# Performance work log

Measured on AMD Instinct MI355X. Metric: run time of the kernel, lower is better.

## Reference

```python
import jax, jax.numpy as jnp
import numpy as np
from jax import lax

DATA_NUM, CNUM, AUG_NUM, LNUM = 64, 6, 4, 3
B, H, W = 16, 512, 512
T_SEL = 0  # fixed aug selection (torch draws np.random.randint at runtime)
EPS = 1e-8
DN = ('NCHW', 'OIHW', 'NCHW')


def setup_inputs() -> dict:
    key = jax.random.key(0)
    ks = jax.random.split(key, 8)
    GLA_img_aug = jax.random.uniform(ks[0], (B, 1, H, W), dtype=jnp.float32)
    lbl = jax.random.randint(ks[1], (B, H, W), 0, CNUM, dtype=jnp.int32)
    index = jax.random.randint(ks[2], (B,), 0, DATA_NUM, dtype=jnp.int32)
    # learned params: Bezier control params (5+2=7 slots, only 0..3 used) and per-(sample,class,aug,layer) tiny conv pairs
    param = jax.random.uniform(ks[3], (DATA_NUM, CNUM, AUG_NUM, LNUM, 7), dtype=jnp.float32)
    w1 = 0.1 * jax.random.normal(ks[4], (DATA_NUM, CNUM, AUG_NUM, LNUM, 4, 1, 3, 3), dtype=jnp.float32)
    b1 = 0.01 * jax.random.normal(ks[5], (DATA_NUM, CNUM, AUG_NUM, LNUM, 4), dtype=jnp.float32)
    w2 = 0.1 * jax.random.normal(ks[6], (DATA_NUM, CNUM, AUG_NUM, LNUM, 1, 4, 3, 3), dtype=jnp.float32)
    b2 = 0.01 * jax.random.normal(ks[7], (DATA_NUM, CNUM, AUG_NUM, LNUM, 1), dtype=jnp.float32)
    return {"GLA_img_aug": GLA_img_aug, "lbl": lbl, "index": index,
            "param": param, "w1": w1, "b1": b1, "w2": w2, "b2": b2}


def _conv_pair(x, w1, b1, w2, b2):
    # x: [1,H,W]; per-sample Conv2d(1,4,3,p=1) -> Conv2d(4,1,3,p=1)
    y = lax.conv_general_dilated(x[None], w1, (1, 1), 'SAME', dimension_numbers=DN) + b1[None, :, None, None]
    y = lax.conv_general_dilated(y, w2, (1, 1), 'SAME', dimension_numbers=DN) + b2[None, :, None, None]
    return y[0]

_conv_batch = jax.vmap(_conv_pair)  # batched over per-sample weights


def _ftransfer(xn, lbl, i, index, param, w1, b1, w2, b2):
    raw = xn                                   # [B,1,H,W]
    mask = (lbl[:, None, :, :] == i)           # [B,1,H,W]
    c = xn * mask
    pp = jax.nn.sigmoid(param[index, i, T_SEL])   # [B,L,7]  (p := sigmoid)
    W1, B1 = w1[index, i, T_SEL], b1[index, i, T_SEL]
    W2, B2 = w2[index, i, T_SEL], b2[index, i, T_SEL]
    for layer in range(LNUM):
        p1 = pp[:, layer, 0][:, None, None, None]
        p2 = pp[:, layer, 1][:, None, None, None]
        p1v = pp[:, layer, 2][:, None, None, None]
        p2v = pp[:, layer, 3][:, None, None, None]
        mix = jax.nn.sigmoid(_conv_batch(raw, W1[:, layer], B1[:, layer], W2[:, layer], B2[:, layer]))
        om = 1.0 - c
        ct = 3.0 * om**2 * c * p1 + 3.0 * om * c**2 * p2 + c**3          # p0=0,  p3=1
        cv = om**3 + 3.0 * om**2 * c * p1v + 3.0 * om * c**2 * p2v       # p0v=1, p3v=0
        c = jnp.clip(ct * mix + cv * (1.0 - mix), 0.0, 1.0)
    # write back only where label == i (equivalent to torch's flag-filtered scatter)
    return jnp.where(mask, c, raw)


def reference(GLA_img_aug, lbl, index, param, w1, b1, w2, b2):
    x = GLA_img_aug
    mn = jnp.min(x, axis=(1, 2, 3), keepdims=True)
    mx = jnp.max(x, axis=(1, 2, 3), keepdims=True)
    scale = mx - mn + EPS
    xn = (x - mn) / scale
    for i in range(CNUM):
        xn = _ftransfer(xn, lbl, i, index, param, w1, b1, w2, b2)
    return xn * scale + mn
```

## Files before the change

kernel.cpp:

```cpp
#include <hip/hip_runtime.h>
#include <stdint.h>

#define HW 512
#define IMG (HW*HW)
#define CNUM_ 6

#define TILE 64
#define HALO 12
#define ST 88
#define SSTR 89
#define NT 512
#define RCAP 256

typedef float f2 __attribute__((ext_vector_type(2)));

#define LTOT 3840

#define RECBASE 2048
#define REC_F 96
#define VARBASE (RECBASE + 96*REC_F)
#define VAR_F 27

__global__ __launch_bounds__(256) void k_prep(const float4* __restrict__ x4,
                       const int* __restrict__ index, const float* __restrict__ param,
                       const float* __restrict__ w1, const float* __restrict__ b1,
                       const float* __restrict__ w2, const float* __restrict__ b2,
                       float* __restrict__ wsf){
    __shared__ float w1s[108], w2s[108], b1s[12], b2s[3], prm[21];
    __shared__ float smn[4], smx[4];
    const int r = blockIdx.x, t = threadIdx.x;
    if (r >= 96){
        int blk = r - 96;
        int base4 = blk * 1024;
        float vmin = 1e30f, vmax = -1e30f;
#pragma unroll
        for (int k = 0; k < 4; k++){
            float4 v = x4[base4 + k*256 + t];
            vmin = fminf(vmin, fminf(fminf(v.x, v.y), fminf(v.z, v.w)));
            vmax = fmaxf(vmax, fmaxf(fmaxf(v.x, v.y), fmaxf(v.z, v.w)));
        }
#pragma unroll
        for (int off = 32; off > 0; off >>= 1){
            vmin = fminf(vmin, __shfl_down(vmin, off));
            vmax = fmaxf(vmax, __shfl_down(vmax, off));
        }
        int wv = t >> 6;
        if ((t & 63) == 0){ smn[wv] = vmin; smx[wv] = vmax; }
        __syncthreads();
        if (t == 0){
            wsf[2*blk]     = fminf(fminf(smn[0], smn[1]), fminf(smn[2], smn[3]));
            wsf[2*blk + 1] = fmaxf(fmaxf(smx[0], smx[1]), fmaxf(smx[2], smx[3]));
        }
        return;
    }
    const int b = r / 6, i = r % 6;
    const int lb0 = (index[b]*CNUM_ + i) * 12;
    if (t < 108){
        int l = t / 36, j = t % 36;
        w1s[t] = w1[(lb0 + l)*36 + j];
        w2s[t] = w2[(lb0 + l)*36 + j];
    }
    if (t < 12) b1s[t] = b1[(lb0 + t/4)*4 + (t%4)];
    if (t < 3)  b2s[t] = b2[lb0 + t];
    if (t < 21) prm[t] = param[(lb0 + t/7)*7 + (t%7)];
    __syncthreads();
    float* rec = wsf + RECBASE + r*REC_F;
    float* var = wsf + VARBASE + r*9*3*VAR_F;
    for (int u = t; u < 9*3*26; u += 256){
        int kind = u / 78, rem = u % 78, l = rem / 26, e = rem % 26;
        int rowk = kind / 3, colk = kind % 3;
        if (e < 25){
            int ty = e/5 - 2, tx = e%5 - 2;
            float we = 0.f;
            for (int d = 0; d < 9; d++){
                int dy = d/3 - 1, dx = d%3 - 1;
                if ((rowk==0 && dy<0)||(rowk==2 && dy>0)||(colk==0 && dx<0)||(colk==2 && dx>0)) continue;
                int ey = ty - dy, ex = tx - dx;
                if (ey < -1 || ey > 1 || ex < -1 || ex > 1) continue;
                for (int c = 0; c < 4; c++)
                    we += w2s[l*36 + c*9 + d] * w1s[l*36 + c*9 + (ey+1)*3 + (ex+1)];
            }
            var[(kind*3 + l)*VAR_F + e] = we;
            if (kind == 4) rec[l*25 + e] = we;
        } else {
            float be = b2s[l];
            for (int c = 0; c < 4; c++){
                float sw = 0.f;
                for (int d = 0; d < 9; d++){
                    int dy = d/3 - 1, dx = d%3 - 1;
                    if ((rowk==0 && dy<0)||(rowk==2 && dy>0)||(colk==0 && dx<0)||(colk==2 && dx>0)) continue;
                    sw += w2s[l*36 + c*9 + d];
                }
                be += b1s[l*4 + c] * sw;
            }
            var[(kind*3 + l)*VAR_F + 25] = be;
            if (kind == 4) rec[75 + l] = be;
        }
    }
    if (t < 18){
        int l = t / 6, q = t % 6;
        float p1  = __builtin_amdgcn_rcpf(1.f + __expf(-prm[l*7 + 0]));
        float p2  = __builtin_amdgcn_rcpf(1.f + __expf(-prm[l*7 + 1]));
        float p1v = __builtin_amdgcn_rcpf(1.f + __expf(-prm[l*7 + 2]));
        float p2v = __builtin_amdgcn_rcpf(1.f + __expf(-prm[l*7 + 3]));
        float v;
        switch (q){
            case 0: v = 3.f*p1; break;
            case 1: v = 3.f*p2 - 6.f*p1; break;
            case 2: v = 1.f + 3.f*p1 - 3.f*p2; break;
            case 3: v = 3.f*p1v - 3.f; break;
            case 4: v = 3.f - 6.f*p1v + 3.f*p2v; break;
            default: v = -1.f + 3.f*p1v - 3.f*p2v; break;
        }
        rec[78 + l*6 + q] = v;
    }
}

__device__ __forceinline__ float sig1(float z){
    return __builtin_amdgcn_rcpf(1.f + __expf(-z));
}

__device__ __forceinline__ float bez3(float c, float mix, const float* __restrict__ cf){
    float ct = c * (cf[0] + c * (cf[1] + c * cf[2]));
    float cv = 1.f + c * (cf[3] + c * (cf[4] + c * cf[5]));
    float r = cv + mix * (ct - cv);
    return __builtin_amdgcn_fmed3f(r, 0.f, 1.f);
}

__device__ __forceinline__ f2 splat(float v){ f2 r = {v, v}; return r; }

__device__ __forceinline__ f2 sig2(f2 z){
    f2 r;
    r.x = __builtin_amdgcn_rcpf(1.f + __expf(-z.x));
    r.y = __builtin_amdgcn_rcpf(1.f + __expf(-z.y));
    return r;
}

__device__ __forceinline__ f2 bez3p(f2 c, f2 mix, const float* __restrict__ cf){
    f2 ct = c * (splat(cf[0]) + c * (splat(cf[1]) + c * splat(cf[2])));
    f2 cv = splat(1.f) + c * (splat(cf[3]) + c * (splat(cf[4]) + c * splat(cf[5])));
    f2 r = cv + mix * (ct - cv);
    r.x = __builtin_amdgcn_fmed3f(r.x, 0.f, 1.f);
    r.y = __builtin_amdgcn_fmed3f(r.y, 0.f, 1.f);
    return r;
}

__device__ __forceinline__ void load_taps(const float* __restrict__ s, int pos, float* tp){
    const float* sp0 = s + pos - (2*SSTR + 2);
    const float* sp1 = s + pos + (SSTR - 2);
#pragma unroll
    for (int wy = 0; wy < 3; wy++)
#pragma unroll
    for (int wx = 0; wx < 5; wx++)
        tp[wy*5 + wx] = sp0[wy*SSTR + wx];
#pragma unroll
    for (int wy = 0; wy < 2; wy++)
#pragma unroll
    for (int wx = 0; wx < 5; wx++)
        tp[15 + wy*5 + wx] = sp1[wy*SSTR + wx];
}

__device__ __forceinline__ void conv_px(const float* __restrict__ s, int pos,
                                        const float* __restrict__ rec,
                                        float& z0, float& z1, float& z2, float& cc){
    float tp[25];
    load_taps(s, pos, tp);
    f2 a0 = {rec[75], 0.f};
    f2 a1 = {rec[76], 0.f};
    f2 a2 = {rec[77], 0.f};
#pragma unroll
    for (int e = 0; e < 24; e += 2){
        f2 tv = {tp[e], tp[e+1]};
        f2 w0 = {rec[e],      rec[e+1]};
        f2 w1 = {rec[25 + e], rec[26 + e]};
        f2 w2 = {rec[50 + e], rec[51 + e]};
        a0 += w0 * tv;
        a1 += w1 * tv;
        a2 += w2 * tv;
    }
    float t24 = tp[24];
    z0 = a0.x + a0.y + rec[24]*t24;
    z1 = a1.x + a1.y + rec[49]*t24;
    z2 = a2.x + a2.y + rec[74]*t24;
    cc = tp[12];
}

__device__ __forceinline__ unsigned short* gl_addr(float* out, int sbase, int Y0, int X0, int e){
    return (unsigned short*)(out + sbase + (Y0 + HALO + (e >> 7))*HW + X0 + HALO) + (e & 127);
}

__device__ __forceinline__ void classify_px(int ce, unsigned short pos, int lane,
        int* cnt, unsigned short* lst, float* out, int sbase, int Y0, int X0){
    unsigned long long m0 = __ballot(ce & 1);
    unsigned long long m1 = __ballot(ce & 2);
    unsigned long long m2 = __ballot(ce & 4);
    int basev = 0;
    if (lane < 6){
        unsigned long long mc = ((lane & 1) ? m0 : ~m0)
                              & ((lane & 2) ? m1 : ~m1)
                              & ((lane & 4) ? m2 : ~m2);
        int pc = __popcll(mc);
        if (pc) basev = atomicAdd(&cnt[lane], pc);
    }
    int mybase = __shfl(basev, ce < 6 ? ce : 0);
    if (ce < 6){
        unsigned long long mself = ((ce & 1) ? m0 : ~m0)
                                 & ((ce & 2) ? m1 : ~m1)
                                 & ((ce & 4) ? m2 : ~m2);
        int p = mybase + __popcll(mself & ((1ull << lane) - 1ull));
        if (ce < 3){
            int capc = 1408 - (ce << 7);
            int offc = ce * (1472 - (ce << 6));
            if (p < capc) lst[offc + p] = pos;
        } else {
            int d = ce - 3;
            int capc = 1056 - 96*d;
            int offc = d * (1104 - 48*d);
            if (p < capc) *gl_addr(out, sbase, Y0, X0, offc + p) = pos;
        }
    }
}

__global__ __launch_bounds__(NT, 8) void k_main(
        const float* __restrict__ x, const int* __restrict__ lbl,
        float* __restrict__ out, const float* __restrict__ wsf){
    __shared__ float s[ST*SSTR];
    __shared__ unsigned short lst[LTOT];
    __shared__ unsigned rlst[RCAP];
    __shared__ int cnt[8];
    __shared__ float snorm[4];
    const int lin = ((blockIdx.z << 3) + blockIdx.y) * 8 + blockIdx.x;
    const int xcd = lin & 7;
    const int e = lin >> 3;
    int img2, idx;
    if (e < 56){
        int r = e >> 1; img2 = e & 1;
        if (r < 8)       idx = r;
        else if (r < 16) idx = 56 + (r - 8);
        else { int t = r - 16; idx = (1 + (t >> 1))*8 + (t & 1)*7; }
    } else {
        int f = e - 56; img2 = f & 1; int t = f >> 1;
        idx = (1 + t/6)*8 + 1 + t%6;
    }
    const int b = xcd*2 + img2;
    const int by = idx >> 3, bx = idx & 7;
    const int X0 = bx * TILE - HALO, Y0 = by * TILE - HALO;
    const int tid = threadIdx.x;
    const int lane = tid & 63;
    const int sbase = b * IMG;
    const bool edgeblk = (bx == 0) | (bx == 7) | (by == 0) | (by == 7);

    if (tid < 8) cnt[tid] = 0;
    if (tid < 64){
        float pmn = wsf[2*(b*64 + tid)];
        float pmx = wsf[2*(b*64 + tid) + 1];
#pragma unroll
        for (int off = 32; off > 0; off >>= 1){
            pmn = fminf(pmn, __shfl_down(pmn, off));
            pmx = fmaxf(pmx, __shfl_down(pmx, off));
        }
        if (tid == 0){
            float scv = pmx - pmn + 1e-8f;
            snorm[0] = pmn; snorm[1] = scv; snorm[2] = 1.0f / scv;
        }
    }
    __syncthreads();
    const float mn = snorm[0], sc = snorm[1], inv = snorm[2];
    const float mninv = mn * inv;

    {
        int q = tid << 2;
        int ly = q / ST, lx = q - ly*ST;
        int pbase = ly*SSTR + lx;
        for (int it = 0; it < 4; it++){
            bool act = (it < 3) | (tid < (ST*ST - 3*4*NT) / 4);
            int gy = Y0 + ly, gxb = X0 + lx;
            bool vq = act & ((unsigned)gy < (unsigned)HW) & ((unsigned)gxb <= (unsigned)(HW - 4));
            float4 xv = {0.f, 0.f, 0.f, 0.f};
            int4  lv = {255, 255, 255, 255};
            if (vq){
                int off = sbase + (gy << 9) + gxb;
                xv = *(const float4*)(x + off);
                lv = *(const int4*)(lbl + off);
                xv.x = xv.x*inv - mninv;
                xv.y = xv.y*inv - mninv;
                xv.z = xv.z*inv - mninv;
                xv.w = xv.w*inv - mninv;
            }
            if (act){
                s[pbase + 0] = xv.x;
                s[pbase + 1] = xv.y;
                s[pbase + 2] = xv.z;
                s[pbase + 3] = xv.w;
            }
            int mrow = min(ly, ST-1-ly);
#pragma unroll
            for (int j = 0; j < 4; j++){
                int c = (&lv.x)[j];
                int lxj = lx + j;
                int margin = min(min(lxj, ST-1-lxj), mrow);
                bool ringj = false;
                if (edgeblk){
                    int gxj = gxb + j;
                    ringj = vq & ((gxj==0) | (gxj==HW-1) | (gy==0) | (gy==HW-1));
                }
                int ce = (c < CNUM_ && !ringj && margin >= 2 + 2*c) ? c : 7;
                classify_px(ce, (unsigned short)(pbase + j), lane, cnt, lst, out, sbase, Y0, X0);
                if (edgeblk){
                    bool ringok = ringj && c < CNUM_ && margin >= 2;
                    unsigned long long rm = __ballot(ringok);
                    if (rm){
                        int base = 0;
                        if (lane == 0) base = atomicAdd(&cnt[6], __popcll(rm));
                        base = __shfl(base, 0);
                        if (ringok){
                            int p = base + __popcll(rm & ((1ull << lane) - 1ull));
                            if (p < RCAP) rlst[p] = ((unsigned)c << 16) | (unsigned)(pbase + j);
                        }
                    }
                }
            }
            lx += 24; ly += 23; pbase += 23*SSTR + 24;
            if (lx >= ST){ lx -= ST; ly += 1; pbase += SSTR - ST; }
        }
    }
    __syncthreads();
    const int rn = min(cnt[6], RCAP);

    unsigned short pf[9];
#pragma unroll
    for (int d = 0; d < 3; d++){
        int capc = 1056 - 96*d;
        int offc = d * (1104 - 48*d);
        int nB = min(cnt[3 + d], capc);
#pragma unroll
        for (int sl = 0; sl < 3; sl++){
            int j = tid + sl*NT;
            unsigned short pv = 0;
            if (j < nB) pv = *gl_addr(out, sbase, Y0, X0, offc + j);
            pf[d*3 + sl] = pv;
        }
    }

#pragma unroll
    for (int cls = 0; cls < CNUM_; cls++){
        const int capc = (cls < 3) ? (1408 - (cls << 7)) : (1056 - 96*(cls - 3));
        const float* rec = wsf + RECBASE + (b*CNUM_ + cls)*REC_F;
        const int n = min(cnt[cls], capc);
        const int j0 = tid, j1 = tid + NT, j2 = tid + 2*NT;
        const bool v0 = j0 < n, v1 = j1 < n, v2 = j2 < n;
        int p0 = 0, p1 = 0, p2 = 0;
        if (cls < 3){
            const unsigned short* lp = lst + cls * (1472 - (cls << 6));
            if (v0) p0 = lp[j0];
            if (v1) p1 = lp[j1];
            if (v2) p2 = lp[j2];
        } else {
            p0 = pf[(cls-3)*3 + 0];
            p1 = pf[(cls-3)*3 + 1];
            p2 = pf[(cls-3)*3 + 2];
        }
        __builtin_amdgcn_s_setprio(1);
        float z00=0.f, z01=0.f, z02=0.f, cc0=0.f;
        float z10=0.f, z11=0.f, z12=0.f, cc1=0.f;
        float u0, u1, u2;
        if (v0) conv_px(s, p0, rec, z00, z01, z02, cc0);
        if (v1) conv_px(s, p1, rec, z10, z11, z12, cc1);
        if (v0 | v1){
            f2 cP = {cc0, cc1};
            cP = bez3p(cP, sig2((f2){z00, z10}), rec + 78);
            cP = bez3p(cP, sig2((f2){z01, z11}), rec + 84);
            cP = bez3p(cP, sig2((f2){z02, z12}), rec + 90);
            u0 = cP.x; u1 = cP.y;
        }
        if (v2){
            float za, zb, zc, cc;
            conv_px(s, p2, rec, za, zb, zc, cc);
            cc = bez3(cc, sig1(za), rec + 78);
            cc = bez3(cc, sig1(zb), rec + 84);
            u2 = bez3(cc, sig1(zc), rec + 90);
        }
        __builtin_amdgcn_s_setprio(0);
        int hav = -1; float rupd = 0.f;
        if (edgeblk && tid < rn){
            unsigned ev = rlst[tid];
            int rc = (int)(ev >> 16), pos = (int)(ev & 0xffff);
            int ly = pos / SSTR, lx = pos % SSTR;
            int margin = min(min(lx, ST-1-lx), min(ly, ST-1-ly));
            if (rc == cls && margin >= 2 + 2*cls){
                int gy = Y0 + ly, gx = X0 + lx;
                int rowk = (gy == 0) ? 0 : ((gy == HW-1) ? 2 : 1);
                int colk = (gx == 0) ? 0 : ((gx == HW-1) ? 2 : 1);
                const float* vb = wsf + VARBASE + ((b*CNUM_ + cls)*9 + rowk*3 + colk)*3*VAR_F;
                float tp[25];
                load_taps(s, pos, tp);
                float c = tp[12];
#pragma unroll
                for (int l = 0; l < 3; l++){
                    float z = vb[l*VAR_F + 25];
#pragma unroll
                    for (int e2 = 0; e2 < 25; e2++) z += vb[l*VAR_F + e2] * tp[e2];
                    c = bez3(c, sig1(z), rec + 78 + 6*l);
                }
                rupd = c; hav = pos;
            }
        }
        __syncthreads();
        if (v0) s[p0] = u0;
        if (v1) s[p1] = u1;
        if (v2) s[p2] = u2;
        if (hav >= 0) s[hav] = rupd;
        __syncthreads();
    }

    for (int j = tid; j < TILE*TILE; j += NT){
        int py = j >> 6, px = j & 63;
        int gy = Y0 + HALO + py, gx = X0 + HALO + px;
        out[sbase + gy*HW + gx] = s[(HALO + py)*SSTR + (HALO + px)] * sc + mn;
    }
}

extern "C" void kernel_launch(void* const* d_in, const int* in_sizes, int n_in,
                              void* d_out, int out_size, void* d_ws, size_t ws_size,
                              hipStream_t stream){
    const float* x     = (const float*)d_in[0];
    const int*   lbl   = (const int*)  d_in[1];
    const int*   index = (const int*)  d_in[2];
    const float* param = (const float*)d_in[3];
    const float* w1    = (const float*)d_in[4];
    const float* b1    = (const float*)d_in[5];
    const float* w2    = (const float*)d_in[6];
    const float* b2    = (const float*)d_in[7];
    float* out = (float*)d_out;
    float* wsf = (float*)d_ws;

    k_prep<<<1120, 256, 0, stream>>>((const float4*)x, index, param, w1, b1, w2, b2, wsf);
    dim3 g(8, 8, 16);
    k_main<<<g, NT, 0, stream>>>(x, lbl, out, wsf);
}
```

Before: 164.1 us.

## Bucket class pixel lists by position mod 32 to get bank-conflict-free gathers

Replaces the ballot-based per-class compaction with a two-pass counting sort. Pixels are binned by class and (pos & 31), the bins are prefix-scanned, then scattered into the class lists, and each lane processes its own bucket. The intent is that lanes in a wave touch stencil positions on distinct LDS banks, cutting bank conflicts in conv_px. The paired f2 conv path is dropped, the RCAP ring buffer is shrunk, and the final store is vectorized to float4. In exchange it adds LDS atomics per pixel, an extra classification pass, and a wavefront loop of up to 6 iterations bounded by the largest bucket, which can cause load imbalance.

```diff
diff --git a/kernel.cpp b/kernel.cpp
--- a/kernel.cpp
+++ b/kernel.cpp
@@ -10,7 +10,7 @@
 #define ST 88
 #define SSTR 89
 #define NT 512
-#define RCAP 256
+#define RCAP 176
 
 typedef float f2 __attribute__((ext_vector_type(2)));
 
@@ -127,24 +127,6 @@
     return __builtin_amdgcn_fmed3f(r, 0.f, 1.f);
 }
 
-__device__ __forceinline__ f2 splat(float v){ f2 r = {v, v}; return r; }
-
-__device__ __forceinline__ f2 sig2(f2 z){
-    f2 r;
-    r.x = __builtin_amdgcn_rcpf(1.f + __expf(-z.x));
-    r.y = __builtin_amdgcn_rcpf(1.f + __expf(-z.y));
-    return r;
-}
-
-__device__ __forceinline__ f2 bez3p(f2 c, f2 mix, const float* __restrict__ cf){
-    f2 ct = c * (splat(cf[0]) + c * (splat(cf[1]) + c * splat(cf[2])));
-    f2 cv = splat(1.f) + c * (splat(cf[3]) + c * (splat(cf[4]) + c * splat(cf[5])));
-    f2 r = cv + mix * (ct - cv);
-    r.x = __builtin_amdgcn_fmed3f(r.x, 0.f, 1.f);
-    r.y = __builtin_amdgcn_fmed3f(r.y, 0.f, 1.f);
-    return r;
-}
-
 __device__ __forceinline__ void load_taps(const float* __restrict__ s, int pos, float* tp){
     const float* sp0 = s + pos - (2*SSTR + 2);
     const float* sp1 = s + pos + (SSTR - 2);
@@ -189,37 +171,8 @@
     return (unsigned short*)(out + sbase + (Y0 + HALO + (e >> 7))*HW + X0 + HALO) + (e & 127);
 }
 
-__device__ __forceinline__ void classify_px(int ce, unsigned short pos, int lane,
-        int* cnt, unsigned short* lst, float* out, int sbase, int Y0, int X0){
-    unsigned long long m0 = __ballot(ce & 1);
-    unsigned long long m1 = __ballot(ce & 2);
-    unsigned long long m2 = __ballot(ce & 4);
-    int basev = 0;
-    if (lane < 6){
-        unsigned long long mc = ((lane & 1) ? m0 : ~m0)
-                              & ((lane & 2) ? m1 : ~m1)
-                              & ((lane & 4) ? m2 : ~m2);
-        int pc = __popcll(mc);
-        if (pc) basev = atomicAdd(&cnt[lane], pc);
-    }
-    int mybase = __shfl(basev, ce < 6 ? ce : 0);
-    if (ce < 6){
-        unsigned long long mself = ((ce & 1) ? m0 : ~m0)
-                                 & ((ce & 2) ? m1 : ~m1)
-                                 & ((ce & 4) ? m2 : ~m2);
-        int p = mybase + __popcll(mself & ((1ull << lane) - 1ull));
-        if (ce < 3){
-            int capc = 1408 - (ce << 7);
-            int offc = ce * (1472 - (ce << 6));
-            if (p < capc) lst[offc + p] = pos;
-        } else {
-            int d = ce - 3;
-            int capc = 1056 - 96*d;
-            int offc = d * (1104 - 48*d);
-            if (p < capc) *gl_addr(out, sbase, Y0, X0, offc + p) = pos;
-        }
-    }
-}
+__device__ __forceinline__ int cls_off(int c){ return c*(1472 - (c << 6)); }
+__device__ __forceinline__ int clsB_off(int d){ return d*(1104 - 48*d); }
 
 __global__ __launch_bounds__(NT, 8) void k_main(
         const float* __restrict__ x, const int* __restrict__ lbl,
@@ -227,6 +180,8 @@
     __shared__ float s[ST*SSTR];
     __shared__ unsigned short lst[LTOT];
     __shared__ unsigned rlst[RCAP];
+    __shared__ unsigned bcnt[192];
+    __shared__ int maxsz[6];
     __shared__ int cnt[8];
     __shared__ float snorm[4];
     const int lin = ((blockIdx.z << 3) + blockIdx.y) * 8 + blockIdx.x;
@@ -247,10 +202,12 @@
     const int X0 = bx * TILE - HALO, Y0 = by * TILE - HALO;
     const int tid = threadIdx.x;
     const int lane = tid & 63;
+    const int wv = tid >> 6;
     const int sbase = b * IMG;
     const bool edgeblk = (bx == 0) | (bx == 7) | (by == 0) | (by == 7);
 
     if (tid < 8) cnt[tid] = 0;
+    if (tid < 192) bcnt[tid] = 0u;
     if (tid < 64){
         float pmn = wsf[2*(b*64 + tid)];
         float pmx = wsf[2*(b*64 + tid) + 1];
@@ -268,12 +225,14 @@
     const float mn = snorm[0], sc = snorm[1], inv = snorm[2];
     const float mninv = mn * inv;
 
+    unsigned c01 = 0, c23 = 0;
     {
         int q = tid << 2;
         int ly = q / ST, lx = q - ly*ST;
         int pbase = ly*SSTR + lx;
+#pragma unroll
         for (int it = 0; it < 4; it++){
-            bool act = (it < 3) | (tid < (ST*ST - 3*4*NT) / 4);
+            bool act = (it < 3) | (tid < 400);
             int gy = Y0 + ly, gxb = X0 + lx;
             bool vq = act & ((unsigned)gy < (unsigned)HW) & ((unsigned)gxb <= (unsigned)(HW - 4));
             float4 xv = {0.f, 0.f, 0.f, 0.f};
@@ -294,6 +253,7 @@
                 s[pbase + 3] = xv.w;
             }
             int mrow = min(ly, ST-1-ly);
+            unsigned cw = 0;
 #pragma unroll
             for (int j = 0; j < 4; j++){
                 int c = (&lv.x)[j];
@@ -305,7 +265,11 @@
                     ringj = vq & ((gxj==0) | (gxj==HW-1) | (gy==0) | (gy==HW-1));
                 }
                 int ce = (c < CNUM_ && !ringj && margin >= 2 + 2*c) ? c : 7;
-                classify_px(ce, (unsigned short)(pbase + j), lane, cnt, lst, out, sbase, Y0, X0);
+                cw |= (unsigned)ce << (j << 2);
+                if (ce < 6){
+                    int pos = pbase + j;
+                    atomicAdd(&bcnt[(ce << 5) + (pos & 31)], 1u);
+                }
                 if (edgeblk){
                     bool ringok = ringj && c < CNUM_ && margin >= 2;
                     unsigned long long rm = __ballot(ringok);
@@ -320,6 +284,8 @@
                     }
                 }
             }
+            if (it < 2) c01 |= cw << ((it & 1) << 4);
+            else        c23 |= cw << ((it & 1) << 4);
             lx += 24; ly += 23; pbase += 23*SSTR + 24;
             if (lx >= ST){ lx -= ST; ly += 1; pbase += SSTR - ST; }
         }
@@ -327,58 +293,83 @@
     __syncthreads();
     const int rn = min(cnt[6], RCAP);
 
-    unsigned short pf[9];
-#pragma unroll
-    for (int d = 0; d < 3; d++){
-        int capc = 1056 - 96*d;
-        int offc = d * (1104 - 48*d);
-        int nB = min(cnt[3 + d], capc);
-#pragma unroll
-        for (int sl = 0; sl < 3; sl++){
-            int j = tid + sl*NT;
-            unsigned short pv = 0;
-            if (j < nB) pv = *gl_addr(out, sbase, Y0, X0, offc + j);
-            pf[d*3 + sl] = pv;
-        }
-    }
-
+    if (tid < 192){
+        int c = tid >> 5, k = tid & 31;
+        int v = (int)bcnt[tid];
+        int mx = v;
+#pragma unroll
+        for (int d = 16; d; d >>= 1) mx = max(mx, __shfl_xor(mx, d, 32));
+        if (k == 0) maxsz[c] = mx;
+        int xsc = v;
+#pragma unroll
+        for (int d = 1; d < 32; d <<= 1){
+            int y = __shfl_up(xsc, d, 32);
+            if (k >= d) xsc += y;
+        }
+        int base = (xsc - v) + ((c < 3) ? cls_off(c) : clsB_off(c - 3));
+        bcnt[tid] = (unsigned)base;
+    }
+    __syncthreads();
+
+    {
+        int q = tid << 2;
+        int ly = q / ST, lx = q - ly*ST;
+        int pbase = ly*SSTR + lx;
+#pragma unroll
+        for (int it = 0; it < 4; it++){
+            unsigned cw = ((it < 2) ? c01 : c23) >> ((it & 1) << 4);
+#pragma unroll
+            for (int j = 0; j < 4; j++){
+                int ce = (int)((cw >> (j << 2)) & 7u);
+                if (ce < 6){
+                    int pos = pbase + j;
+                    int slot = (int)atomicAdd(&bcnt[(ce << 5) + (pos & 31)], 1u);
+                    if (ce < 3){
+                        if (slot < cls_off(ce) + 1408 - (ce << 7))
+                            lst[slot] = (unsigned short)pos;
+                    } else {
+                        int d = ce - 3;
+                        if (slot < clsB_off(d) + 1056 - 96*d)
+                            *gl_addr(out, sbase, Y0, X0, slot) = (unsigned short)pos;
+                    }
+                }
+            }
+            lx += 24; ly += 23; pbase += 23*SSTR + 24;
+            if (lx >= ST){ lx -= ST; ly += 1; pbase += SSTR - ST; }
+        }
+    }
+    __syncthreads();
+
+    const int kk = lane & 31, half = lane >> 5;
 #pragma unroll
     for (int cls = 0; cls < CNUM_; cls++){
-        const int capc = (cls < 3) ? (1408 - (cls << 7)) : (1056 - 96*(cls - 3));
         const float* rec = wsf + RECBASE + (b*CNUM_ + cls)*REC_F;
-        const int n = min(cnt[cls], capc);
-        const int j0 = tid, j1 = tid + NT, j2 = tid + 2*NT;
-        const bool v0 = j0 < n, v1 = j1 < n, v2 = j2 < n;
-        int p0 = 0, p1 = 0, p2 = 0;
-        if (cls < 3){
-            const unsigned short* lp = lst + cls * (1472 - (cls << 6));
-            if (v0) p0 = lp[j0];
-            if (v1) p1 = lp[j1];
-            if (v2) p2 = lp[j2];
-        } else {
-            p0 = pf[(cls-3)*3 + 0];
-            p1 = pf[(cls-3)*3 + 1];
-            p2 = pf[(cls-3)*3 + 2];
-        }
+        const int tb = (cls << 5) + kk;
+        const int endk = (int)bcnt[tb];
+        const int basek = kk ? (int)bcnt[tb - 1]
+                             : ((cls < 3) ? cls_off(cls) : clsB_off(cls - 3));
+        const int msz = maxsz[cls];
+        float us[6]; int ps[6];
         __builtin_amdgcn_s_setprio(1);
-        float z00=0.f, z01=0.f, z02=0.f, cc0=0.f;
-        float z10=0.f, z11=0.f, z12=0.f, cc1=0.f;
-        float u0, u1, u2;
-        if (v0) conv_px(s, p0, rec, z00, z01, z02, cc0);
-        if (v1) conv_px(s, p1, rec, z10, z11, z12, cc1);
-        if (v0 | v1){
-            f2 cP = {cc0, cc1};
-            cP = bez3p(cP, sig2((f2){z00, z10}), rec + 78);
-            cP = bez3p(cP, sig2((f2){z01, z11}), rec + 84);
-            cP = bez3p(cP, sig2((f2){z02, z12}), rec + 90);
-            u0 = cP.x; u1 = cP.y;
-        }
-        if (v2){
-            float za, zb, zc, cc;
-            conv_px(s, p2, rec, za, zb, zc, cc);
-            cc = bez3(cc, sig1(za), rec + 78);
-            cc = bez3(cc, sig1(zb), rec + 84);
-            u2 = bez3(cc, sig1(zc), rec + 90);
+#pragma unroll
+        for (int m = 0; m < 6; m++){
+            ps[m] = 0; us[m] = 0.f;
+            int g = wv + (m << 3);
+            if (g + g < msz){
+                int idxe = basek + g + g + half;
+                bool va = idxe < endk;
+                int pos = 0;
+                if (va) pos = (cls < 3) ? (int)lst[idxe]
+                                        : (int)*gl_addr(out, sbase, Y0, X0, idxe);
+                if (va){
+                    float z0, z1, z2, cc;
+                    conv_px(s, pos, rec, z0, z1, z2, cc);
+                    cc = bez3(cc, sig1(z0), rec + 78);
+                    cc = bez3(cc, sig1(z1), rec + 84);
+                    us[m] = bez3(cc, sig1(z2), rec + 90);
+                    ps[m] = pos;
+                }
+            }
         }
         __builtin_amdgcn_s_setprio(0);
         int hav = -1; float rupd = 0.f;
@@ -406,17 +397,19 @@
             }
         }
         __syncthreads();
-        if (v0) s[p0] = u0;
-        if (v1) s[p1] = u1;
-        if (v2) s[p2] = u2;
+#pragma unroll
+        for (int m = 0; m < 6; m++) if (ps[m]) s[ps[m]] = us[m];
         if (hav >= 0) s[hav] = rupd;
         __syncthreads();
     }
 
-    for (int j = tid; j < TILE*TILE; j += NT){
-        int py = j >> 6, px = j & 63;
-        int gy = Y0 + HALO + py, gx = X0 + HALO + px;
-        out[sbase + gy*HW + gx] = s[(HALO + py)*SSTR + (HALO + px)] * sc + mn;
+    for (int j = tid; j < 1024; j += NT){
+        int py = j >> 4, px4 = (j & 15) << 2;
+        const float* sp = s + (HALO + py)*SSTR + HALO + px4;
+        float4 o;
+        o.x = sp[0]*sc + mn; o.y = sp[1]*sc + mn;
+        o.z = sp[2]*sc + mn; o.w = sp[3]*sc + mn;
+        *(float4*)(out + sbase + ((Y0 + HALO + py) << 9) + X0 + HALO + px4) = o;
     }
 }
 
```

Measured after the change: 170.9 us. 4.2% more time.
